# Performance work log

Measured on AMD Instinct MI355X. Metric: run time of the kernel, lower is better.

Reference implementation:

```python
import jax, jax.numpy as jnp
import numpy as np

N_HEADS = 16
R = 256.0


def setup_inputs() -> dict:
    key = jax.random.key(0)
    ks = jax.random.split(key, 8)
    B, T, D, H = 4, 1024, 1024, N_HEADS
    s = 1.0 / np.sqrt(D)
    return {
        "x": jax.random.normal(ks[0], (B, T, D), jnp.float32),
        "Wq": jax.random.normal(ks[1], (D, D), jnp.float32) * s,
        "Wk": jax.random.normal(ks[2], (D, D), jnp.float32) * s,
        "Wv": jax.random.normal(ks[3], (D, D), jnp.float32) * s,
        "Wo": jax.random.normal(ks[4], (D, D), jnp.float32) * s,
        "bo": jnp.zeros((D,), jnp.float32),
        "Wspan": jax.random.normal(ks[5], (H, D), jnp.float32) * s,
        "bspan": jnp.zeros((H,), jnp.float32),
    }


def reference(x, Wq, Wk, Wv, Wo, bo, Wspan, bspan):
    B, T, D = x.shape
    H = N_HEADS
    dh = D // H
    scale = jnp.sqrt(jnp.float32(dh))

    # projections -> (B, H, T, dh)
    def proj(W):
        return jnp.einsum('btd,ed->bte', x, W).reshape(B, T, H, dh).transpose(0, 2, 1, 3)
    Q, K, V = proj(Wq), proj(Wk), proj(Wv)

    # learned span per head: z = T * sigmoid(span_net(mean_t x))  -> (B, H)
    z = T * jax.nn.sigmoid(jnp.einsum('bd,hd->bh', x.mean(axis=1), Wspan) + bspan)

    idx = jnp.arange(T, dtype=jnp.float32)
    dist = idx[None, :] - idx[:, None]          # dist[i,j] = j - i
    causal = dist >= 0                           # matches torch code's mask
    dist_c = jnp.maximum(dist, 0.0)

    scores = jnp.einsum('bhtd,bhsd->bhts', Q, K) / scale
    scores = jnp.where(causal[None, None], scores, -jnp.inf)
    attn = jax.nn.softmax(scores, axis=-1)

    # soft span mask chi_z(h) = clamp((R + z - dist)/R, 0, 1)  (Eq 7)
    span_mask = jnp.clip((R + z[:, :, None, None] - dist_c[None, None]) / R, 0.0, 1.0)
    attn = attn * span_mask
    attn = attn / (attn.sum(axis=-1, keepdims=True) + 1e-8)
    # dropout p=0.0 (eval) -> identity

    out = jnp.einsum('bhts,bhsd->bhtd', attn, V)
    out = out.transpose(0, 2, 1, 3).reshape(B, T, D)
    return jnp.einsum('btd,ed->bte', out, Wo) + bo
```

## Files before the change

kernel.cpp:

```cpp
#include <hip/hip_runtime.h>

#define T_SEQ 1024
#define D_MODEL 1024
#define NH 16
#define DH 64
#define R_SPAN 256.0f

typedef unsigned short ushort_t;
typedef __attribute__((ext_vector_type(8))) short bf16x8;
typedef __attribute__((ext_vector_type(4))) float f32x4;

__device__ __forceinline__ ushort_t f2bf(float f){
  union { float f; unsigned u; } v; v.f = f;
  unsigned r = v.u + 0x7fffu + ((v.u >> 16) & 1u);
  return (ushort_t)(r >> 16);
}

__device__ __forceinline__ ushort_t f2bf_fast(float f){
  union { float f; unsigned u; } v; v.f = f;
  return (ushort_t)((v.u + 0x8000u) >> 16);
}

__device__ __forceinline__ float fast_exp2(float x){
#if __has_builtin(__builtin_amdgcn_exp2f)
  return __builtin_amdgcn_exp2f(x);
#else
  return __expf(x * 0.69314718056f);
#endif
}

typedef __attribute__((address_space(1))) void GV;
typedef __attribute__((address_space(3))) void LV;
__device__ __forceinline__ void gld16(const void* g, void* l){
  __builtin_amdgcn_global_load_lds((GV*)g, (LV*)l, 16, 0, 0);
}

__global__ void conv_all(const float* __restrict__ x,
                         const float* s1, const float* s2, const float* s3, const float* s4,
                         ushort_t* __restrict__ x_bf, ushort_t* __restrict__ w_bf){
  const int chunk = blockIdx.y;
  const float* src;
  ushort_t* dst;
  if (chunk < 4){
    src = x + ((size_t)chunk << 20);
    dst = x_bf + ((size_t)chunk << 20);
  } else {
    const float* ws[4] = {s1, s2, s3, s4};
    src = ws[chunk - 4];
    dst = w_bf + ((size_t)(chunk - 4) << 20);
  }
  const int i = (blockIdx.x * 256 + threadIdx.x) * 4;
  float4 v = *(const float4*)(src + i);
  ushort4 o; o.x = f2bf(v.x); o.y = f2bf(v.y); o.z = f2bf(v.z); o.w = f2bf(v.w);
  *(ushort4*)(dst + i) = o;
}

__global__ void mean_kernel(const float* __restrict__ x, float* __restrict__ xmean){
  const int b = blockIdx.y, d0 = blockIdx.x * 64;
  const int dl = threadIdx.x & 63, tg = threadIdx.x >> 6;
  const float* p = x + (size_t)b * T_SEQ * D_MODEL + d0 + dl;
  float s = 0.f;
  for (int t = tg * 256; t < tg * 256 + 256; ++t) s += p[(size_t)t * D_MODEL];
  __shared__ float red[4][64];
  red[tg][dl] = s;
  __syncthreads();
  if (tg == 0){
    float tot = red[0][dl] + red[1][dl] + red[2][dl] + red[3][dl];
    xmean[b * D_MODEL + d0 + dl] = tot * (1.0f / T_SEQ);
  }
}

__global__ void span_kernel(const float* __restrict__ xmean, const float* __restrict__ Wspan,
                            const float* __restrict__ bspan, float* __restrict__ z){
  const int h = blockIdx.x, b = blockIdx.y, l = threadIdx.x;
  const float* xm = xmean + b * D_MODEL;
  const float* wv = Wspan + h * D_MODEL;
  float s = 0.f;
  for (int i = l; i < D_MODEL; i += 64) s += xm[i] * wv[i];
  for (int off = 32; off; off >>= 1) s += __shfl_down(s, off, 64);
  if (l == 0){
    float logit = s + bspan[h];
    z[b * NH + h] = (float)T_SEQ / (1.0f + __expf(-logit));
  }
}

template<int FP32OUT>
__global__ __launch_bounds__(256) void gemm_bt(
    const ushort_t* __restrict__ A,
    const ushort_t* __restrict__ B,
    void* __restrict__ C,
    const float* __restrict__ bias,
    const int M, const int N, const int K)
{
  __shared__ ushort_t At[2][128 * 32];
  __shared__ ushort_t Bt[2][128 * 32];

  const int z = blockIdx.z;
  const ushort_t* Bz = B + (size_t)z * N * K;

  const int tid = threadIdx.x;
  const int w = tid >> 6, lane = tid & 63;
  const int q = lane >> 4, c = lane & 15;
  const int m0 = blockIdx.y * 128, n0 = blockIdx.x * 128;
  const int wm = (w >> 1) * 64, wn = (w & 1) * 64;

  const int lr = lane >> 2;
  const int lc = (lane & 3) * 8;

  f32x4 acc[4][4] = {};

  const ushort_t* ga0 = A  + (size_t)(m0 + w * 16 + lr) * K + lc;
  const ushort_t* gb0 = Bz + (size_t)(n0 + w * 16 + lr) * K + lc;

  const int S = K >> 5;
  gld16(ga0,                   &At[0][(w * 16) * 32]);
  gld16(ga0 + (size_t)64 * K,  &At[0][(64 + w * 16) * 32]);
  gld16(gb0,                   &Bt[0][(w * 16) * 32]);
  gld16(gb0 + (size_t)64 * K,  &Bt[0][(64 + w * 16) * 32]);

  for (int s = 0; s < S; ++s){
    __syncthreads();
    if (s + 1 < S){
      const int k0 = (s + 1) << 5;
      const int nb = (s + 1) & 1;
      gld16(ga0 + k0,                   &At[nb][(w * 16) * 32]);
      gld16(ga0 + (size_t)64 * K + k0,  &At[nb][(64 + w * 16) * 32]);
      gld16(gb0 + k0,                   &Bt[nb][(w * 16) * 32]);
      gld16(gb0 + (size_t)64 * K + k0,  &Bt[nb][(64 + w * 16) * 32]);
    }
    const ushort_t* at = At[s & 1];
    const ushort_t* bt = Bt[s & 1];

    bf16x8 af[4], bfv[4];
#pragma unroll
    for (int i = 0; i < 4; ++i) af[i]  = *(const bf16x8*)&at[(wm + i * 16 + c) * 32 + q * 8];
#pragma unroll
    for (int j = 0; j < 4; ++j) bfv[j] = *(const bf16x8*)&bt[(wn + j * 16 + c) * 32 + q * 8];
#pragma unroll
    for (int i = 0; i < 4; ++i)
#pragma unroll
      for (int j = 0; j < 4; ++j)
        acc[i][j] = __builtin_amdgcn_mfma_f32_16x16x32_bf16(af[i], bfv[j], acc[i][j], 0, 0, 0);
  }

  if (FP32OUT){
#pragma unroll
    for (int i = 0; i < 4; ++i){
#pragma unroll
      for (int j = 0; j < 4; ++j){
        const int row = m0 + wm + i * 16 + q * 4;
        const int col = n0 + wn + j * 16 + c;
#pragma unroll
        for (int r = 0; r < 4; ++r)
          ((float*)C)[(size_t)(row + r) * N + col] = acc[i][j][r] + bias[col];
      }
    }
  } else if (z == 2){
    ushort_t* Cv = (ushort_t*)C + (size_t)2 * M * N;
    const int bb = m0 >> 10;
#pragma unroll
    for (int i = 0; i < 4; ++i){
#pragma unroll
      for (int j = 0; j < 4; ++j){
        const int col = n0 + wn + j * 16 + c;
        const int t0 = (m0 & 1023) + wm + i * 16 + q * 4;
        ushort4 pk;
        pk.x = f2bf_fast(acc[i][j][0]); pk.y = f2bf_fast(acc[i][j][1]);
        pk.z = f2bf_fast(acc[i][j][2]); pk.w = f2bf_fast(acc[i][j][3]);
        *(ushort4*)&Cv[((size_t)bb << 20) + (size_t)col * 1024 + t0] = pk;
      }
    }
  } else {
#pragma unroll
    for (int i = 0; i < 4; ++i){
#pragma unroll
      for (int j = 0; j < 4; ++j){
        const int row = m0 + wm + i * 16 + q * 4;
        const int col = n0 + wn + j * 16 + c;
#pragma unroll
        for (int r = 0; r < 4; ++r)
          ((ushort_t*)C + (size_t)z * M * N)[(size_t)(row + r) * N + col] = f2bf_fast(acc[i][j][r]);
      }
    }
  }
}

#define LP 72
__global__ __launch_bounds__(512) void attn_kernel(
    const ushort_t* __restrict__ Qg,
    const ushort_t* __restrict__ Kg,
    const ushort_t* __restrict__ Vtg,
    const float* __restrict__ zspan,
    ushort_t* __restrict__ Og)
{
  __shared__ ushort_t Qs[128 * LP];
  __shared__ ushort_t Ks[64 * LP];
  __shared__ ushort_t Vt[64 * LP];
  __shared__ ushort_t Ps[8][16 * LP];

  const int id = blockIdx.x;
  const int qt = (id >> 3) & 7;
  const int g  = ((id >> 6) << 3) | (id & 7);
  const int b = g >> 4, h = g & 15;
  const int q0 = qt * 128;
  const int tid = threadIdx.x, w = tid >> 6, lane = tid & 63;
  const int q = lane >> 4, c = lane & 15;

  const size_t base = ((size_t)b * T_SEQ) * D_MODEL + (size_t)h * DH;
  const ushort_t* vtb = Vtg + ((size_t)b << 20) + ((size_t)h << 16);

  {
    const int row = tid >> 2, seg = tid & 3;
    const uint4* gq = (const uint4*)(Qg + base + (size_t)(q0 + row) * D_MODEL);
    uint4* qs = (uint4*)&Qs[row * LP];
    qs[seg * 2]     = gq[seg * 2];
    qs[seg * 2 + 1] = gq[seg * 2 + 1];
  }

  const float zz = zspan[b * NH + h];
  const int jend = min(T_SEQ, (int)(q0 + 127 + R_SPAN + zz) + 1);

  float d1[4] = {0, 0, 0, 0};
  f32x4 o[4] = {};

  const int wi0 = q0 + w * 16, wi1 = wi0 + 15;
  int i_row[4];
  float ar[4];
#pragma unroll
  for (int r = 0; r < 4; ++r){
    i_row[r] = wi0 + q * 4 + r;
    ar[r] = (R_SPAN + zz + (float)i_row[r]) * (1.0f / R_SPAN);
  }
  const float kexp = 0.125f * 1.44269504f;

  const int srow = tid >> 3, sseg = tid & 7;
  const ushort_t* kg = Kg + base + sseg * 8;
  const ushort_t* vg = vtb + (size_t)srow * 1024 + sseg * 8;

  uint4 kreg = *(const uint4*)(kg + (size_t)(q0 + srow) * D_MODEL);
  uint4 vreg = *(const uint4*)(vg + q0);

  for (int j0 = q0; j0 < jend; j0 += 64){
    __syncthreads();
    *(uint4*)&Ks[srow * LP + sseg * 8] = kreg;
    *(uint4*)&Vt[srow * LP + sseg * 8] = vreg;
    if (j0 + 64 < jend){
      kreg = *(const uint4*)(kg + (size_t)(j0 + 64 + srow) * D_MODEL);
      vreg = *(const uint4*)(vg + j0 + 64);
    }
    __syncthreads();

    if (j0 + 63 < wi0) continue;
    if ((float)(j0 - wi1) > R_SPAN + zz) continue;

    f32x4 s[4] = {};
    {
      bf16x8 aq0 = *(const bf16x8*)&Qs[(w * 16 + c) * LP + q * 8];
      bf16x8 aq1 = *(const bf16x8*)&Qs[(w * 16 + c) * LP + 32 + q * 8];
#pragma unroll
      for (int jf = 0; jf < 4; ++jf){
        bf16x8 bk0 = *(const bf16x8*)&Ks[(jf * 16 + c) * LP + q * 8];
        s[jf] = __builtin_amdgcn_mfma_f32_16x16x32_bf16(aq0, bk0, s[jf], 0, 0, 0);
        bf16x8 bk1 = *(const bf16x8*)&Ks[(jf * 16 + c) * LP + 32 + q * 8];
        s[jf] = __builtin_amdgcn_mfma_f32_16x16x32_bf16(aq1, bk1, s[jf], 0, 0, 0);
      }
    }

    const bool need_mask = (j0 <= wi1);
    const bool full = ((float)(j0 + 63 - wi0) <= zz);

    if (full){
      if (need_mask){
#pragma unroll
        for (int jf = 0; jf < 4; ++jf){
          const int j = j0 + jf * 16 + c;
#pragma unroll
          for (int r = 0; r < 4; ++r){
            float p = fast_exp2(s[jf][r] * kexp);
            p = (j >= i_row[r]) ? p : 0.f;
            d1[r] += p;
            Ps[w][(q * 4 + r) * LP + jf * 16 + c] = f2bf_fast(p);
          }
        }
      } else {
#pragma unroll
        for (int jf = 0; jf < 4; ++jf){
#pragma unroll
          for (int r = 0; r < 4; ++r){
            float p = fast_exp2(s[jf][r] * kexp);
            d1[r] += p;
            Ps[w][(q * 4 + r) * LP + jf * 16 + c] = f2bf_fast(p);
          }
        }
      }
    } else {
      float fjR[4];
#pragma unroll
      for (int jf = 0; jf < 4; ++jf) fjR[jf] = (float)(j0 + jf * 16 + c) * (1.0f / R_SPAN);
      if (need_mask){
#pragma unroll
        for (int jf = 0; jf < 4; ++jf){
          const int j = j0 + jf * 16 + c;
#pragma unroll
          for (int r = 0; r < 4; ++r){
            float p = fast_exp2(s[jf][r] * kexp);
            p = (j >= i_row[r]) ? p : 0.f;
            float chi = fminf(fmaxf(ar[r] - fjR[jf], 0.f), 1.f);
            float pc = p * chi;
            d1[r] += pc;
            Ps[w][(q * 4 + r) * LP + jf * 16 + c] = f2bf_fast(pc);
          }
        }
      } else {
#pragma unroll
        for (int jf = 0; jf < 4; ++jf){
#pragma unroll
          for (int r = 0; r < 4; ++r){
            float p = fast_exp2(s[jf][r] * kexp);
            float chi = fminf(fmaxf(ar[r] - fjR[jf], 0.f), 1.f);
            float pc = p * chi;
            d1[r] += pc;
            Ps[w][(q * 4 + r) * LP + jf * 16 + c] = f2bf_fast(pc);
          }
        }
      }
    }

    {
      bf16x8 pa0 = *(const bf16x8*)&Ps[w][c * LP + q * 8];
      bf16x8 pa1 = *(const bf16x8*)&Ps[w][c * LP + 32 + q * 8];
#pragma unroll
      for (int nf = 0; nf < 4; ++nf){
        bf16x8 bv0 = *(const bf16x8*)&Vt[(nf * 16 + c) * LP + q * 8];
        o[nf] = __builtin_amdgcn_mfma_f32_16x16x32_bf16(pa0, bv0, o[nf], 0, 0, 0);
        bf16x8 bv1 = *(const bf16x8*)&Vt[(nf * 16 + c) * LP + 32 + q * 8];
        o[nf] = __builtin_amdgcn_mfma_f32_16x16x32_bf16(pa1, bv1, o[nf], 0, 0, 0);
      }
    }
  }

#pragma unroll
  for (int r = 0; r < 4; ++r){
    float a1 = d1[r];
    a1 += __shfl_xor(a1, 1, 64);
    a1 += __shfl_xor(a1, 2, 64);
    a1 += __shfl_xor(a1, 4, 64);
    a1 += __shfl_xor(a1, 8, 64);
    const float inv = 1.0f / (a1 + 1e-20f);
    const size_t rowbase = base + (size_t)i_row[r] * D_MODEL;
#pragma unroll
    for (int nf = 0; nf < 4; ++nf){
      Og[rowbase + nf * 16 + c] = f2bf_fast(o[nf][r] * inv);
    }
  }
}

extern "C" void kernel_launch(void* const* d_in, const int* in_sizes, int n_in,
                              void* d_out, int out_size, void* d_ws, size_t ws_size,
                              hipStream_t stream)
{
  const float* x     = (const float*)d_in[0];
  const float* Wq    = (const float*)d_in[1];
  const float* Wk    = (const float*)d_in[2];
  const float* Wv    = (const float*)d_in[3];
  const float* Wo    = (const float*)d_in[4];
  const float* bo    = (const float*)d_in[5];
  const float* Wspan = (const float*)d_in[6];
  const float* bspan = (const float*)d_in[7];

  const size_t MT = (size_t)4 * T_SEQ;

  ushort_t* x_bf = (ushort_t*)d_ws;
  ushort_t* w_bf = x_bf + MT * D_MODEL;
  ushort_t* qkv  = w_bf + (size_t)4 * D_MODEL * D_MODEL;
  ushort_t* attn = qkv + (size_t)3 * MT * D_MODEL;
  float* xmean   = (float*)(attn + MT * D_MODEL);
  float* zsp     = xmean + 4 * D_MODEL;

  conv_all<<<dim3(1024, 8), 256, 0, stream>>>(x, Wq, Wk, Wv, Wo, x_bf, w_bf);
  mean_kernel<<<dim3(16, 4), 256, 0, stream>>>(x, xmean);
  span_kernel<<<dim3(16, 4), 64, 0, stream>>>(xmean, Wspan, bspan, zsp);

  gemm_bt<0><<<dim3(8, 32, 3), 256, 0, stream>>>(x_bf, w_bf, qkv, nullptr, 4096, 1024, 1024);

  attn_kernel<<<dim3(512), 512, 0, stream>>>(qkv, qkv + MT * D_MODEL,
                                             qkv + 2 * MT * D_MODEL, zsp, attn);

  gemm_bt<1><<<dim3(8, 32, 1), 256, 0, stream>>>(attn, w_bf + (size_t)3 * D_MODEL * D_MODEL,
                                                 d_out, bo, 4096, 1024, 1024);
}
```

Baseline: 198.5 us.

## Fuse x fp32-to-bf16 conversion into QKV GEMM and widen attention KV tiles

The separate conversion of x to bf16 is removed. The QKV GEMM now loads fp32 A tiles into registers, converts them and stores them to LDS, with a one-stage register prefetch. This drops a 16MB write and read pass, but the QKV GEMM now reads x in fp32 three times (once per z slice) and loses the async global-to-LDS path for A. Separately, the attention kernel stages 128 keys per iteration as two 64-wide halves, halving the number of barriers, and hoists the Q fragments out of the loop, at the cost of more LDS.

```diff
diff --git a/kernel.cpp b/kernel.cpp
--- a/kernel.cpp
+++ b/kernel.cpp
@@ -35,20 +35,11 @@
   __builtin_amdgcn_global_load_lds((GV*)g, (LV*)l, 16, 0, 0);
 }
 
-__global__ void conv_all(const float* __restrict__ x,
-                         const float* s1, const float* s2, const float* s3, const float* s4,
-                         ushort_t* __restrict__ x_bf, ushort_t* __restrict__ w_bf){
-  const int chunk = blockIdx.y;
-  const float* src;
-  ushort_t* dst;
-  if (chunk < 4){
-    src = x + ((size_t)chunk << 20);
-    dst = x_bf + ((size_t)chunk << 20);
-  } else {
-    const float* ws[4] = {s1, s2, s3, s4};
-    src = ws[chunk - 4];
-    dst = w_bf + ((size_t)(chunk - 4) << 20);
-  }
+__global__ void conv_w(const float* s1, const float* s2, const float* s3, const float* s4,
+                       ushort_t* __restrict__ w_bf){
+  const float* ws[4] = {s1, s2, s3, s4};
+  const float* src = ws[blockIdx.y];
+  ushort_t* dst = w_bf + ((size_t)blockIdx.y << 20);
   const int i = (blockIdx.x * 256 + threadIdx.x) * 4;
   float4 v = *(const float4*)(src + i);
   ushort4 o; o.x = f2bf(v.x); o.y = f2bf(v.y); o.z = f2bf(v.z); o.w = f2bf(v.w);
@@ -84,9 +75,9 @@
   }
 }
 
-template<int FP32OUT>
+template<int FP32OUT, int AFP32>
 __global__ __launch_bounds__(256) void gemm_bt(
-    const ushort_t* __restrict__ A,
+    const void* __restrict__ Ap,
     const ushort_t* __restrict__ B,
     void* __restrict__ C,
     const float* __restrict__ bias,
@@ -109,12 +100,33 @@
 
   f32x4 acc[4][4] = {};
 
-  const ushort_t* ga0 = A  + (size_t)(m0 + w * 16 + lr) * K + lc;
+  const float*    Ax = (const float*)Ap;
+  const ushort_t* Ab = (const ushort_t*)Ap;
+
+  const ushort_t* ga0 = Ab + (size_t)(m0 + w * 16 + lr) * K + lc;
   const ushort_t* gb0 = Bz + (size_t)(n0 + w * 16 + lr) * K + lc;
 
+  const int ar = tid >> 3, ac = (tid & 7) * 4;
+
   const int S = K >> 5;
-  gld16(ga0,                   &At[0][(w * 16) * 32]);
-  gld16(ga0 + (size_t)64 * K,  &At[0][(64 + w * 16) * 32]);
+  float4 a4[4];
+
+  if (AFP32){
+#pragma unroll
+    for (int rr = 0; rr < 4; ++rr){
+      float4 v = *(const float4*)(Ax + (size_t)(m0 + rr * 32 + ar) * K + ac);
+      ushort4 o; o.x = f2bf(v.x); o.y = f2bf(v.y); o.z = f2bf(v.z); o.w = f2bf(v.w);
+      *(ushort4*)&At[0][(rr * 32 + ar) * 32 + ac] = o;
+    }
+    if (S > 1){
+#pragma unroll
+      for (int rr = 0; rr < 4; ++rr)
+        a4[rr] = *(const float4*)(Ax + (size_t)(m0 + rr * 32 + ar) * K + 32 + ac);
+    }
+  } else {
+    gld16(ga0,                   &At[0][(w * 16) * 32]);
+    gld16(ga0 + (size_t)64 * K,  &At[0][(64 + w * 16) * 32]);
+  }
   gld16(gb0,                   &Bt[0][(w * 16) * 32]);
   gld16(gb0 + (size_t)64 * K,  &Bt[0][(64 + w * 16) * 32]);
 
@@ -123,8 +135,23 @@
     if (s + 1 < S){
       const int k0 = (s + 1) << 5;
       const int nb = (s + 1) & 1;
-      gld16(ga0 + k0,                   &At[nb][(w * 16) * 32]);
-      gld16(ga0 + (size_t)64 * K + k0,  &At[nb][(64 + w * 16) * 32]);
+      if (AFP32){
+#pragma unroll
+        for (int rr = 0; rr < 4; ++rr){
+          ushort4 o; o.x = f2bf(a4[rr].x); o.y = f2bf(a4[rr].y);
+          o.z = f2bf(a4[rr].z); o.w = f2bf(a4[rr].w);
+          *(ushort4*)&At[nb][(rr * 32 + ar) * 32 + ac] = o;
+        }
+        if (s + 2 < S){
+          const int k2 = (s + 2) << 5;
+#pragma unroll
+          for (int rr = 0; rr < 4; ++rr)
+            a4[rr] = *(const float4*)(Ax + (size_t)(m0 + rr * 32 + ar) * K + k2 + ac);
+        }
+      } else {
+        gld16(ga0 + k0,                   &At[nb][(w * 16) * 32]);
+        gld16(ga0 + (size_t)64 * K + k0,  &At[nb][(64 + w * 16) * 32]);
+      }
       gld16(gb0 + k0,                   &Bt[nb][(w * 16) * 32]);
       gld16(gb0 + (size_t)64 * K + k0,  &Bt[nb][(64 + w * 16) * 32]);
     }
@@ -185,7 +212,8 @@
   }
 }
 
-#define LP 72
+#define LPQ 72
+#define VP 136
 __global__ __launch_bounds__(512) void attn_kernel(
     const ushort_t* __restrict__ Qg,
     const ushort_t* __restrict__ Kg,
@@ -193,10 +221,10 @@
     const float* __restrict__ zspan,
     ushort_t* __restrict__ Og)
 {
-  __shared__ ushort_t Qs[128 * LP];
-  __shared__ ushort_t Ks[64 * LP];
-  __shared__ ushort_t Vt[64 * LP];
-  __shared__ ushort_t Ps[8][16 * LP];
+  __shared__ ushort_t Qs[128 * LPQ];
+  __shared__ ushort_t Ks[128 * LPQ];
+  __shared__ ushort_t Vt[64 * VP];
+  __shared__ ushort_t Ps[8][16 * LPQ];
 
   const int id = blockIdx.x;
   const int qt = (id >> 3) & 7;
@@ -212,10 +240,13 @@
   {
     const int row = tid >> 2, seg = tid & 3;
     const uint4* gq = (const uint4*)(Qg + base + (size_t)(q0 + row) * D_MODEL);
-    uint4* qs = (uint4*)&Qs[row * LP];
+    uint4* qs = (uint4*)&Qs[row * LPQ];
     qs[seg * 2]     = gq[seg * 2];
     qs[seg * 2 + 1] = gq[seg * 2 + 1];
   }
+  __syncthreads();
+  const bf16x8 aq0 = *(const bf16x8*)&Qs[(w * 16 + c) * LPQ + q * 8];
+  const bf16x8 aq1 = *(const bf16x8*)&Qs[(w * 16 + c) * LPQ + 32 + q * 8];
 
   const float zz = zspan[b * NH + h];
   const int jend = min(T_SEQ, (int)(q0 + 127 + R_SPAN + zz) + 1);
@@ -225,116 +256,124 @@
 
   const int wi0 = q0 + w * 16, wi1 = wi0 + 15;
   int i_row[4];
-  float ar[4];
+  float ar4[4];
 #pragma unroll
   for (int r = 0; r < 4; ++r){
     i_row[r] = wi0 + q * 4 + r;
-    ar[r] = (R_SPAN + zz + (float)i_row[r]) * (1.0f / R_SPAN);
+    ar4[r] = (R_SPAN + zz + (float)i_row[r]) * (1.0f / R_SPAN);
   }
   const float kexp = 0.125f * 1.44269504f;
 
-  const int srow = tid >> 3, sseg = tid & 7;
-  const ushort_t* kg = Kg + base + sseg * 8;
-  const ushort_t* vg = vtb + (size_t)srow * 1024 + sseg * 8;
-
-  uint4 kreg = *(const uint4*)(kg + (size_t)(q0 + srow) * D_MODEL);
-  uint4 vreg = *(const uint4*)(vg + q0);
-
-  for (int j0 = q0; j0 < jend; j0 += 64){
+  const int krow = tid >> 2, kseg = (tid & 3) * 16;
+  const int vrow = tid >> 3, vseg = (tid & 7) * 16;
+  const ushort_t* kgp = Kg + base + kseg;
+  const ushort_t* vgp = vtb + (size_t)vrow * 1024 + vseg;
+
+  uint4 ka = *(const uint4*)(kgp + (size_t)(q0 + krow) * D_MODEL);
+  uint4 kb = *(const uint4*)(kgp + (size_t)(q0 + krow) * D_MODEL + 8);
+  uint4 va = *(const uint4*)(vgp + q0);
+  uint4 vb = *(const uint4*)(vgp + q0 + 8);
+
+  for (int j0 = q0; j0 < jend; j0 += 128){
     __syncthreads();
-    *(uint4*)&Ks[srow * LP + sseg * 8] = kreg;
-    *(uint4*)&Vt[srow * LP + sseg * 8] = vreg;
-    if (j0 + 64 < jend){
-      kreg = *(const uint4*)(kg + (size_t)(j0 + 64 + srow) * D_MODEL);
-      vreg = *(const uint4*)(vg + j0 + 64);
+    *(uint4*)&Ks[krow * LPQ + kseg]     = ka;
+    *(uint4*)&Ks[krow * LPQ + kseg + 8] = kb;
+    *(uint4*)&Vt[vrow * VP + vseg]      = va;
+    *(uint4*)&Vt[vrow * VP + vseg + 8]  = vb;
+    if (j0 + 128 < jend){
+      ka = *(const uint4*)(kgp + (size_t)(j0 + 128 + krow) * D_MODEL);
+      kb = *(const uint4*)(kgp + (size_t)(j0 + 128 + krow) * D_MODEL + 8);
+      va = *(const uint4*)(vgp + j0 + 128);
+      vb = *(const uint4*)(vgp + j0 + 128 + 8);
     }
     __syncthreads();
 
-    if (j0 + 63 < wi0) continue;
-    if ((float)(j0 - wi1) > R_SPAN + zz) continue;
-
-    f32x4 s[4] = {};
-    {
-      bf16x8 aq0 = *(const bf16x8*)&Qs[(w * 16 + c) * LP + q * 8];
-      bf16x8 aq1 = *(const bf16x8*)&Qs[(w * 16 + c) * LP + 32 + q * 8];
+#pragma unroll
+    for (int hh = 0; hh < 2; ++hh){
+      const int j0h = j0 + hh * 64;
+      if (j0h >= jend) break;
+      if (j0h + 63 < wi0) continue;
+      if ((float)(j0h - wi1) > R_SPAN + zz) continue;
+
+      f32x4 s[4] = {};
 #pragma unroll
       for (int jf = 0; jf < 4; ++jf){
-        bf16x8 bk0 = *(const bf16x8*)&Ks[(jf * 16 + c) * LP + q * 8];
+        bf16x8 bk0 = *(const bf16x8*)&Ks[(hh * 64 + jf * 16 + c) * LPQ + q * 8];
         s[jf] = __builtin_amdgcn_mfma_f32_16x16x32_bf16(aq0, bk0, s[jf], 0, 0, 0);
-        bf16x8 bk1 = *(const bf16x8*)&Ks[(jf * 16 + c) * LP + 32 + q * 8];
+        bf16x8 bk1 = *(const bf16x8*)&Ks[(hh * 64 + jf * 16 + c) * LPQ + 32 + q * 8];
         s[jf] = __builtin_amdgcn_mfma_f32_16x16x32_bf16(aq1, bk1, s[jf], 0, 0, 0);
       }
-    }
-
-    const bool need_mask = (j0 <= wi1);
-    const bool full = ((float)(j0 + 63 - wi0) <= zz);
-
-    if (full){
-      if (need_mask){
-#pragma unroll
-        for (int jf = 0; jf < 4; ++jf){
-          const int j = j0 + jf * 16 + c;
-#pragma unroll
-          for (int r = 0; r < 4; ++r){
-            float p = fast_exp2(s[jf][r] * kexp);
-            p = (j >= i_row[r]) ? p : 0.f;
-            d1[r] += p;
-            Ps[w][(q * 4 + r) * LP + jf * 16 + c] = f2bf_fast(p);
+
+      const bool need_mask = (j0h <= wi1);
+      const bool full = ((float)(j0h + 63 - wi0) <= zz);
+
+      if (full){
+        if (need_mask){
+#pragma unroll
+          for (int jf = 0; jf < 4; ++jf){
+            const int j = j0h + jf * 16 + c;
+#pragma unroll
+            for (int r = 0; r < 4; ++r){
+              float p = fast_exp2(s[jf][r] * kexp);
+              p = (j >= i_row[r]) ? p : 0.f;
+              d1[r] += p;
+              Ps[w][(q * 4 + r) * LPQ + jf * 16 + c] = f2bf_fast(p);
+            }
+          }
+        } else {
+#pragma unroll
+          for (int jf = 0; jf < 4; ++jf){
+#pragma unroll
+            for (int r = 0; r < 4; ++r){
+              float p = fast_exp2(s[jf][r] * kexp);
+              d1[r] += p;
+              Ps[w][(q * 4 + r) * LPQ + jf * 16 + c] = f2bf_fast(p);
+            }
           }
         }
       } else {
-#pragma unroll
-        for (int jf = 0; jf < 4; ++jf){
-#pragma unroll
-          for (int r = 0; r < 4; ++r){
-            float p = fast_exp2(s[jf][r] * kexp);
-            d1[r] += p;
-            Ps[w][(q * 4 + r) * LP + jf * 16 + c] = f2bf_fast(p);
+        float fjR[4];
+#pragma unroll
+        for (int jf = 0; jf < 4; ++jf) fjR[jf] = (float)(j0h + jf * 16 + c) * (1.0f / R_SPAN);
+        if (need_mask){
+#pragma unroll
+          for (int jf = 0; jf < 4; ++jf){
+            const int j = j0h + jf * 16 + c;
+#pragma unroll
+            for (int r = 0; r < 4; ++r){
+              float p = fast_exp2(s[jf][r] * kexp);
+              p = (j >= i_row[r]) ? p : 0.f;
+              float chi = fminf(fmaxf(ar4[r] - fjR[jf], 0.f), 1.f);
+              float pc = p * chi;
+              d1[r] += pc;
+              Ps[w][(q * 4 + r) * LPQ + jf * 16 + c] = f2bf_fast(pc);
+            }
+          }
+        } else {
+#pragma unroll
+          for (int jf = 0; jf < 4; ++jf){
+#pragma unroll
+            for (int r = 0; r < 4; ++r){
+              float p = fast_exp2(s[jf][r] * kexp);
+              float chi = fminf(fmaxf(ar4[r] - fjR[jf], 0.f), 1.f);
+              float pc = p * chi;
+              d1[r] += pc;
+              Ps[w][(q * 4 + r) * LPQ + jf * 16 + c] = f2bf_fast(pc);
+            }
           }
         }
       }
-    } else {
-      float fjR[4];
-#pragma unroll
-      for (int jf = 0; jf < 4; ++jf) fjR[jf] = (float)(j0 + jf * 16 + c) * (1.0f / R_SPAN);
-      if (need_mask){
-#pragma unroll
-        for (int jf = 0; jf < 4; ++jf){
-          const int j = j0 + jf * 16 + c;
-#pragma unroll
-          for (int r = 0; r < 4; ++r){
-            float p = fast_exp2(s[jf][r] * kexp);
-            p = (j >= i_row[r]) ? p : 0.f;
-            float chi = fminf(fmaxf(ar[r] - fjR[jf], 0.f), 1.f);
-            float pc = p * chi;
-            d1[r] += pc;
-            Ps[w][(q * 4 + r) * LP + jf * 16 + c] = f2bf_fast(pc);
-          }
+
+      {
+        bf16x8 pa0 = *(const bf16x8*)&Ps[w][c * LPQ + q * 8];
+        bf16x8 pa1 = *(const bf16x8*)&Ps[w][c * LPQ + 32 + q * 8];
+#pragma unroll
+        for (int nf = 0; nf < 4; ++nf){
+          bf16x8 bv0 = *(const bf16x8*)&Vt[(nf * 16 + c) * VP + hh * 64 + q * 8];
+          o[nf] = __builtin_amdgcn_mfma_f32_16x16x32_bf16(pa0, bv0, o[nf], 0, 0, 0);
+          bf16x8 bv1 = *(const bf16x8*)&Vt[(nf * 16 + c) * VP + hh * 64 + 32 + q * 8];
+          o[nf] = __builtin_amdgcn_mfma_f32_16x16x32_bf16(pa1, bv1, o[nf], 0, 0, 0);
         }
-      } else {
-#pragma unroll
-        for (int jf = 0; jf < 4; ++jf){
-#pragma unroll
-          for (int r = 0; r < 4; ++r){
-            float p = fast_exp2(s[jf][r] * kexp);
-            float chi = fminf(fmaxf(ar[r] - fjR[jf], 0.f), 1.f);
-            float pc = p * chi;
-            d1[r] += pc;
-            Ps[w][(q * 4 + r) * LP + jf * 16 + c] = f2bf_fast(pc);
-          }
-        }
-      }
-    }
-
-    {
-      bf16x8 pa0 = *(const bf16x8*)&Ps[w][c * LP + q * 8];
-      bf16x8 pa1 = *(const bf16x8*)&Ps[w][c * LP + 32 + q * 8];
-#pragma unroll
-      for (int nf = 0; nf < 4; ++nf){
-        bf16x8 bv0 = *(const bf16x8*)&Vt[(nf * 16 + c) * LP + q * 8];
-        o[nf] = __builtin_amdgcn_mfma_f32_16x16x32_bf16(pa0, bv0, o[nf], 0, 0, 0);
-        bf16x8 bv1 = *(const bf16x8*)&Vt[(nf * 16 + c) * LP + 32 + q * 8];
-        o[nf] = __builtin_amdgcn_mfma_f32_16x16x32_bf16(pa1, bv1, o[nf], 0, 0, 0);
       }
     }
   }
@@ -370,22 +409,21 @@
 
   const size_t MT = (size_t)4 * T_SEQ;
 
-  ushort_t* x_bf = (ushort_t*)d_ws;
-  ushort_t* w_bf = x_bf + MT * D_MODEL;
+  ushort_t* w_bf = (ushort_t*)d_ws;
   ushort_t* qkv  = w_bf + (size_t)4 * D_MODEL * D_MODEL;
   ushort_t* attn = qkv + (size_t)3 * MT * D_MODEL;
   float* xmean   = (float*)(attn + MT * D_MODEL);
   float* zsp     = xmean + 4 * D_MODEL;
 
-  conv_all<<<dim3(1024, 8), 256, 0, stream>>>(x, Wq, Wk, Wv, Wo, x_bf, w_bf);
+  conv_w<<<dim3(1024, 4), 256, 0, stream>>>(Wq, Wk, Wv, Wo, w_bf);
   mean_kernel<<<dim3(16, 4), 256, 0, stream>>>(x, xmean);
   span_kernel<<<dim3(16, 4), 64, 0, stream>>>(xmean, Wspan, bspan, zsp);
 
-  gemm_bt<0><<<dim3(8, 32, 3), 256, 0, stream>>>(x_bf, w_bf, qkv, nullptr, 4096, 1024, 1024);
+  gemm_bt<0, 1><<<dim3(8, 32, 3), 256, 0, stream>>>(x, w_bf, qkv, nullptr, 4096, 1024, 1024);
 
   attn_kernel<<<dim3(512), 512, 0, stream>>>(qkv, qkv + MT * D_MODEL,
                                              qkv + 2 * MT * D_MODEL, zsp, attn);
 
-  gemm_bt<1><<<dim3(8, 32, 1), 256, 0, stream>>>(attn, w_bf + (size_t)3 * D_MODEL * D_MODEL,
-                                                 d_out, bo, 4096, 1024, 1024);
-}
+  gemm_bt<1, 0><<<dim3(8, 32, 1), 256, 0, stream>>>(attn, w_bf + (size_t)3 * D_MODEL * D_MODEL,
+                                                    d_out, bo, 4096, 1024, 1024);
+}
```

Measured after the change: 205.8 us. +3.6%, slower.
